# Kernel tuning notes

Measured on AMD Instinct MI355X. Metric: run time of the kernel, lower is better.

The kernel has to match this reference:

```python
import jax, jax.numpy as jnp
import numpy as np

HEADS = 8
HDIM = 64
MAX_PEMB = 512


def setup_inputs() -> dict:
    key = jax.random.key(0)
    ks = jax.random.split(key, 6)
    B, S, D = 4, 1024, 512
    return {
        "x": jax.random.normal(ks[0], (B, S, D), jnp.float32),
        "attn_mask": jnp.ones((B, S), jnp.bool_),
        "Wq": jax.random.normal(ks[1], (D, HEADS * HDIM), jnp.float32) * 0.02,
        "Wkv": jax.random.normal(ks[2], (D, 2 * HEADS * HDIM), jnp.float32) * 0.02,
        "Wout": jax.random.normal(ks[3], (HEADS * HDIM, D), jnp.float32) * 0.02,
        "bout": jnp.zeros((D,), jnp.float32),
        "pemb": jax.random.normal(ks[4], (2 * MAX_PEMB + 1, HDIM), jnp.float32) * 0.02,
    }


def reference(x, attn_mask, Wq, Wkv, Wout, bout, pemb):
    # attn_mask is unpacked but unused in the original call(); faithful to source.
    B, S, D = x.shape
    scale = HDIM ** (-0.5)

    q = (x @ Wq).reshape(B, S, HEADS, HDIM).transpose(0, 2, 1, 3)  # [B,H,S,hd]
    kv = x @ Wkv
    k, v = jnp.split(kv, 2, axis=-1)
    k = k.reshape(B, S, HEADS, HDIM).transpose(0, 2, 1, 3)
    v = v.reshape(B, S, HEADS, HDIM).transpose(0, 2, 1, 3)

    attn_score = jnp.einsum('bhqd,bhkd->bhqk', q, k) * scale

    seq = jnp.arange(S)
    dist = jnp.clip(seq[:, None] - seq[None, :], -MAX_PEMB, MAX_PEMB) + MAX_PEMB  # [S,S]
    rel_pemb = pemb[dist]  # [S,S,hd]
    pos_attn = jnp.einsum('bhsd,std->bhst', q, rel_pemb) * scale  # [B,H,S,S]

    attn_probs = jax.nn.softmax(attn_score + pos_attn, axis=-1)
    ctx = jnp.einsum('bhqk,bhkd->bqhd', attn_probs, v).reshape(B, S, HEADS * HDIM)
    return ctx @ Wout + bout
```

## Files before the change

### kernel.cpp

```cpp
#include <hip/hip_runtime.h>
#include <hip/hip_bf16.h>

constexpr int BATCH = 4;
constexpr int SEQ   = 1024;
constexpr int DM    = 512;
constexpr int NH    = 8;
constexpr int HD    = 64;
constexpr int NQKV  = 1536;

typedef unsigned short u16;
typedef __attribute__((ext_vector_type(8))) __bf16 bf8;
typedef __attribute__((ext_vector_type(4))) float  f4;

#define MFMA16(a, b, c) __builtin_amdgcn_mfma_f32_16x16x32_bf16(a, b, c, 0, 0, 0)

#define QSC 0.18033688f

static __device__ __forceinline__ u16 f2b(float f) {
    union { float f; unsigned u; } v; v.f = f;
    unsigned r = v.u + 0x7FFFu + ((v.u >> 16) & 1u);
    return (u16)(r >> 16);
}
static __device__ __forceinline__ float fexp2(float x) {
    return __builtin_amdgcn_exp2f(x);
}
static __device__ __forceinline__ void gl_lds16(const void* g, void* l) {
    __builtin_amdgcn_global_load_lds(
        (const __attribute__((address_space(1))) void*)g,
        (__attribute__((address_space(3))) void*)l, 16, 0, 0);
}

__device__ __forceinline__ void tcvt_tile(const float* __restrict__ in,
                                          u16* __restrict__ out,
                                          int R, int C, int bx, int by, int tid,
                                          float (*t)[33]) {
    int r0 = by * 32, c0 = bx * 32;
    int lc = tid & 31, lr = tid >> 5;
    #pragma unroll
    for (int p = 0; p < 4; p++) {
        int r = lr + p * 8;
        t[r][lc] = in[(size_t)(r0 + r) * C + c0 + lc];
    }
    __syncthreads();
    #pragma unroll
    for (int p = 0; p < 4; p++) {
        int r = lr + p * 8;
        out[(size_t)(c0 + r) * R + r0 + lc] = f2b(t[lc][r]);
    }
}

__global__ __launch_bounds__(256)
void prep(const float* __restrict__ x, const float* __restrict__ Wq,
          const float* __restrict__ Wkv, const float* __restrict__ Wout,
          const float* __restrict__ pemb,
          u16* __restrict__ xb, u16* __restrict__ qkvw,
          u16* __restrict__ Woutt, u16* __restrict__ pembb) {
    __shared__ float t[32][33];
    const int blk = blockIdx.x, tid = threadIdx.x;
    if (blk < 2048) {
        int i = (blk * 256 + tid) * 4;
        float4 v = *(const float4*)(x + i);
        ushort4 o = {f2b(v.x), f2b(v.y), f2b(v.z), f2b(v.w)};
        *(ushort4*)(xb + i) = o;
    } else if (blk < 2113) {
        int i = ((blk - 2048) * 256 + tid) * 4;
        if (i < 1025 * HD) {
            float4 v = *(const float4*)(pemb + i);
            ushort4 o = {f2b(v.x), f2b(v.y), f2b(v.z), f2b(v.w)};
            *(ushort4*)(pembb + i) = o;
        }
    } else if (blk < 2369) {
        int l = blk - 2113;
        tcvt_tile(Wq, qkvw, 512, 512, l & 15, l >> 4, tid, t);
    } else if (blk < 2881) {
        int l = blk - 2369;
        tcvt_tile(Wkv, qkvw + 512 * 512, 512, 1024, l & 31, l >> 5, tid, t);
    } else {
        int l = blk - 2881;
        tcvt_tile(Wout, Woutt, 512, 512, l & 15, l >> 4, tid, t);
    }
}

__global__ __launch_bounds__(256)
void gemm_bt(const u16* __restrict__ A, const u16* __restrict__ Bt,
             int M, int N, int K,
             float* __restrict__ Cf, const float* __restrict__ bias,
             __bf16* __restrict__ qtb, __bf16* __restrict__ ktb,
             __bf16* __restrict__ vtb) {
    __shared__ __align__(16) u16 As[2][64][32];
    __shared__ __align__(16) u16 Bs[2][128][32];
    const int tid = threadIdx.x, w = tid >> 6, lane = tid & 63;
    const int l15 = lane & 15, l4 = lane >> 4;
    const int wr = (w >> 1) * 32, wc = (w & 1) * 64;
    const int bm = blockIdx.y * 64, bn = blockIdx.x * 128;

    f4 acc[2][4];
    #pragma unroll
    for (int i = 0; i < 2; i++)
        #pragma unroll
        for (int j = 0; j < 4; j++) acc[i][j] = (f4){0.f, 0.f, 0.f, 0.f};

    const int rS = lane >> 2;
    const int cS = (lane & 3) * 8;

    for (int k0 = 0; k0 < K; k0 += 64) {
        #pragma unroll
        for (int ks = 0; ks < 2; ks++) {
            gl_lds16(A + (size_t)(bm + w * 16 + rS) * K + k0 + ks * 32 + cS,
                     &As[ks][w * 16][0]);
            gl_lds16(Bt + (size_t)(bn + w * 32 + rS) * K + k0 + ks * 32 + cS,
                     &Bs[ks][w * 32][0]);
            gl_lds16(Bt + (size_t)(bn + w * 32 + 16 + rS) * K + k0 + ks * 32 + cS,
                     &Bs[ks][w * 32 + 16][0]);
        }
        __syncthreads();
        #pragma unroll
        for (int ks = 0; ks < 2; ks++) {
            bf8 af[2], bf[4];
            #pragma unroll
            for (int i = 0; i < 2; i++)
                af[i] = *(const bf8*)&As[ks][wr + i * 16 + l15][l4 * 8];
            #pragma unroll
            for (int j = 0; j < 4; j++)
                bf[j] = *(const bf8*)&Bs[ks][wc + j * 16 + l15][l4 * 8];
            #pragma unroll
            for (int i = 0; i < 2; i++)
                #pragma unroll
                for (int j = 0; j < 4; j++)
                    acc[i][j] = MFMA16(af[i], bf[j], acc[i][j]);
        }
        __syncthreads();
    }
    #pragma unroll
    for (int i = 0; i < 2; i++)
        #pragma unroll
        for (int j = 0; j < 4; j++) {
            const int col = bn + wc + j * 16 + l15;
            const int row0 = bm + wr + i * 16 + l4 * 4;
            if (Cf) {
                #pragma unroll
                for (int reg = 0; reg < 4; reg++)
                    Cf[(size_t)(row0 + reg) * N + col] = acc[i][j][reg] + bias[col];
            } else if (col < 512) {
                int h = col >> 6, d = col & 63;
                #pragma unroll
                for (int reg = 0; reg < 4; reg++) {
                    int row = row0 + reg;
                    int b = row >> 10, t = row & 1023;
                    qtb[((((size_t)(b * 8 + h)) << 10 | t) << 6) | d] =
                        (__bf16)(acc[i][j][reg] * QSC);
                }
            } else if (col < 1024) {
                int h = (col >> 6) - 8, d = col & 63;
                #pragma unroll
                for (int reg = 0; reg < 4; reg++) {
                    int row = row0 + reg;
                    int b = row >> 10, t = row & 1023;
                    ktb[((((size_t)(b * 8 + h)) << 10 | t) << 6) | d] =
                        (__bf16)acc[i][j][reg];
                }
            } else {
                int h = (col >> 6) - 16, d = col & 63;
                int b = row0 >> 10, t = row0 & 1023;
                __bf16 pk[4];
                #pragma unroll
                for (int reg = 0; reg < 4; reg++) pk[reg] = (__bf16)acc[i][j][reg];
                *(ushort4*)&vtb[(((size_t)(b * 8 + h) * 64 + d) << 10) | t] =
                    *(ushort4*)pk;
            }
        }
}

__global__ __launch_bounds__(256)
void attn_mfma(const u16* __restrict__ qtb, const u16* __restrict__ ktb,
               const u16* __restrict__ vtb, const u16* __restrict__ pembb,
               __bf16* __restrict__ ctxb) {
    __shared__ __align__(16) __bf16 Kb[2][64][72];
    __shared__ __align__(16) __bf16 Vb[2][64][72];
    __shared__ __align__(16) __bf16 Ps[64][72];
    __shared__ __align__(16) __bf16 Qd[64][136];

    const int tid = threadIdx.x, w = tid >> 6, lane = tid & 63;
    const int l15 = lane & 15, l4 = lane >> 4;
    const int bh = blockIdx.x, b = bh >> 3;
    const int s0 = blockIdx.y * 64;

    const u16* qp = qtb + ((size_t)bh * SEQ + s0 + w * 16 + l15) * HD + l4 * 8;
    bf8 qa0 = *(const bf8*)qp;
    bf8 qa1 = *(const bf8*)(qp + 32);

    #pragma unroll
    for (int pass = 0; pass < 2; pass++) {
        const int jlo = s0 + 449 + pass * 64;
        #pragma unroll
        for (int jt = 0; jt < 4; jt++) {
            int jc = min(1024, max(0, jlo + jt * 16 + l15));
            const u16* pp = pembb + (size_t)jc * HD + l4 * 8;
            bf8 b0 = *(const bf8*)pp;
            bf8 b1 = *(const bf8*)(pp + 32);
            f4 f = (f4){0.f, 0.f, 0.f, 0.f};
            f = MFMA16(qa0, b0, f);
            f = MFMA16(qa1, b1, f);
            int sl = w * 16 + l4 * 4;
            int j = jlo + jt * 16 + l15;
            #pragma unroll
            for (int reg = 0; reg < 4; reg++)
                Qd[sl + reg][j & 127] = (__bf16)f[reg];
        }
    }
    asm volatile("" ::: "memory");

    float l_r[4] = {0.f, 0.f, 0.f, 0.f};
    f4 o[4];
    #pragma unroll
    for (int dt = 0; dt < 4; dt++) o[dt] = (f4){0.f, 0.f, 0.f, 0.f};

    const u16* kbase = ktb + (size_t)bh * SEQ * HD;
    const u16* vbase = vtb + (size_t)bh * HD * SEQ;
    const u16* pbase = pembb + l4 * 8;

    const int sr = tid >> 3, sc = (tid & 7) * 8;

    *(bf8*)&Kb[0][sr][sc]      = *(const bf8*)(kbase + (size_t)sr * HD + sc);
    *(bf8*)&Kb[0][sr + 32][sc] = *(const bf8*)(kbase + (size_t)(sr + 32) * HD + sc);
    *(bf8*)&Vb[0][sr][sc]      = *(const bf8*)(vbase + (size_t)sr * SEQ + sc);
    *(bf8*)&Vb[0][sr + 32][sc] = *(const bf8*)(vbase + (size_t)(sr + 32) * SEQ + sc);
    __syncthreads();

    for (int i = 0; i < 16; i++) {
        const int cur = i & 1, nxt = cur ^ 1;
        const int t0 = i * 64, t1 = t0 + 64;
        const bool pre = (i < 15);
        bf8 kr0, kr1, vr0, vr1, pb0[4], pb1[4];
        const int jlo_next = s0 + 449 - 64 * (i + 1);
        if (pre) {
            kr0 = *(const bf8*)(kbase + (size_t)(t1 + sr) * HD + sc);
            kr1 = *(const bf8*)(kbase + (size_t)(t1 + sr + 32) * HD + sc);
            vr0 = *(const bf8*)(vbase + (size_t)sr * SEQ + t1 + sc);
            vr1 = *(const bf8*)(vbase + (size_t)(sr + 32) * SEQ + t1 + sc);
            #pragma unroll
            for (int jt = 0; jt < 4; jt++) {
                int jc = min(1024, max(0, jlo_next + jt * 16 + l15));
                const u16* pp = pbase + (size_t)jc * HD;
                pb0[jt] = *(const bf8*)pp;
                pb1[jt] = *(const bf8*)(pp + 32);
            }
        }

        f4 s[4];
        #pragma unroll
        for (int jt = 0; jt < 4; jt++) {
            bf8 b0 = *(const bf8*)&Kb[cur][jt * 16 + l15][l4 * 8];
            bf8 b1 = *(const bf8*)&Kb[cur][jt * 16 + l15][32 + l4 * 8];
            f4 acc = (f4){0.f, 0.f, 0.f, 0.f};
            acc = MFMA16(qa0, b0, acc);
            acc = MFMA16(qa1, b1, acc);
            s[jt] = acc;
        }
        const int jbase = s0 - t0 + 512;
        float sc4[4][4];
        #pragma unroll
        for (int jt = 0; jt < 4; jt++) {
            int tl = jt * 16 + l15;
            #pragma unroll
            for (int reg = 0; reg < 4; reg++) {
                int sl = w * 16 + l4 * 4 + reg;
                int j = jbase + sl - tl;
                float p = fexp2(s[jt][reg] + (float)Qd[sl][j & 127]);
                sc4[jt][reg] = p;
                l_r[reg] += p;
            }
        }
        #pragma unroll
        for (int jt = 0; jt < 4; jt++)
            #pragma unroll
            for (int reg = 0; reg < 4; reg++)
                Ps[w * 16 + l4 * 4 + reg][jt * 16 + l15] = (__bf16)sc4[jt][reg];
        asm volatile("" ::: "memory");
        bf8 pa0 = *(const bf8*)&Ps[w * 16 + l15][l4 * 8];
        bf8 pa1 = *(const bf8*)&Ps[w * 16 + l15][32 + l4 * 8];
        #pragma unroll
        for (int dt = 0; dt < 4; dt++) {
            bf8 v0 = *(const bf8*)&Vb[cur][dt * 16 + l15][l4 * 8];
            bf8 v1 = *(const bf8*)&Vb[cur][dt * 16 + l15][32 + l4 * 8];
            o[dt] = MFMA16(pa0, v0, o[dt]);
            o[dt] = MFMA16(pa1, v1, o[dt]);
        }
        if (pre) {
            #pragma unroll
            for (int jt = 0; jt < 4; jt++) {
                f4 f = (f4){0.f, 0.f, 0.f, 0.f};
                f = MFMA16(qa0, pb0[jt], f);
                f = MFMA16(qa1, pb1[jt], f);
                int j = jlo_next + jt * 16 + l15;
                #pragma unroll
                for (int reg = 0; reg < 4; reg++)
                    Qd[w * 16 + l4 * 4 + reg][j & 127] = (__bf16)f[reg];
            }
            *(bf8*)&Kb[nxt][sr][sc]      = kr0;
            *(bf8*)&Kb[nxt][sr + 32][sc] = kr1;
            *(bf8*)&Vb[nxt][sr][sc]      = vr0;
            *(bf8*)&Vb[nxt][sr + 32][sc] = vr1;
        }
        __syncthreads();
    }
    #pragma unroll
    for (int reg = 0; reg < 4; reg++) {
        float r2 = l_r[reg];
        #pragma unroll
        for (int off = 8; off; off >>= 1) r2 += __shfl_xor(r2, off);
        l_r[reg] = 1.f / r2;
    }
    const int h = bh & 7;
    #pragma unroll
    for (int dt = 0; dt < 4; dt++)
        #pragma unroll
        for (int reg = 0; reg < 4; reg++) {
            int srow = s0 + w * 16 + l4 * 4 + reg;
            float v = o[dt][reg] * l_r[reg];
            ctxb[(size_t)(b * SEQ + srow) * DM + h * HD + dt * 16 + l15] = (__bf16)v;
        }
}

extern "C" void kernel_launch(void* const* d_in, const int* in_sizes, int n_in,
                              void* d_out, int out_size, void* d_ws, size_t ws_size,
                              hipStream_t stream) {
    const float* x    = (const float*)d_in[0];
    const float* Wq   = (const float*)d_in[2];
    const float* Wkv  = (const float*)d_in[3];
    const float* Wout = (const float*)d_in[4];
    const float* bout = (const float*)d_in[5];
    const float* pemb = (const float*)d_in[6];
    float* out = (float*)d_out;

    const int M = BATCH * SEQ;
    u16* p = (u16*)d_ws;
    u16* xb    = p; p += (size_t)M * DM;
    u16* qkvw  = p; p += (size_t)NQKV * DM;
    u16* Woutt = p; p += (size_t)DM * DM;
    u16* pembb = p; p += (size_t)1025 * HD;
    u16* qtb   = p; p += (size_t)M * DM;
    u16* ktb   = p; p += (size_t)M * DM;
    u16* vtb   = p; p += (size_t)M * DM;
    u16* ctxb  = p; p += (size_t)M * DM;

    prep<<<3137, 256, 0, stream>>>(x, Wq, Wkv, Wout, pemb, xb, qkvw, Woutt, pembb);

    gemm_bt<<<dim3(NQKV / 128, M / 64), 256, 0, stream>>>(
        xb, qkvw, M, NQKV, DM, nullptr, nullptr,
        (__bf16*)qtb, (__bf16*)ktb, (__bf16*)vtb);

    attn_mfma<<<dim3(BATCH * NH, SEQ / 64), 256, 0, stream>>>(
        qtb, ktb, vtb, pembb, (__bf16*)ctxb);

    gemm_bt<<<dim3(DM / 128, M / 64), 256, 0, stream>>>(
        ctxb, Woutt, M, DM, DM, out, bout, nullptr, nullptr, nullptr);
}
```

Before: 135.5 us.

## Load V fragments straight from global, swizzle P tile, deepen GEMM K-step

In the attention kernel, the V tile is no longer staged through shared memory. Each wave now loads its MFMA B-operand fragments for V directly from global memory on every iteration, which removes the Vb buffers and their LDS stores and reads. The P tile in shared memory now uses an XOR swizzle on columns to cut bank conflicts between the row-wise writes and the fragment reads. The QKV/out GEMM now stages 128 K-elements per barrier instead of 64, halving the number of syncs at the cost of twice the LDS footprint. The direct V loads are redundant across the four waves and are issued late, so they may expose global latency.

```diff
diff --git a/kernel.cpp b/kernel.cpp
--- a/kernel.cpp
+++ b/kernel.cpp
@@ -87,8 +87,8 @@
              float* __restrict__ Cf, const float* __restrict__ bias,
              __bf16* __restrict__ qtb, __bf16* __restrict__ ktb,
              __bf16* __restrict__ vtb) {
-    __shared__ __align__(16) u16 As[2][64][32];
-    __shared__ __align__(16) u16 Bs[2][128][32];
+    __shared__ __align__(16) u16 As[4][64][32];
+    __shared__ __align__(16) u16 Bs[4][128][32];
     const int tid = threadIdx.x, w = tid >> 6, lane = tid & 63;
     const int l15 = lane & 15, l4 = lane >> 4;
     const int wr = (w >> 1) * 32, wc = (w & 1) * 64;
@@ -103,9 +103,9 @@
     const int rS = lane >> 2;
     const int cS = (lane & 3) * 8;
 
-    for (int k0 = 0; k0 < K; k0 += 64) {
-        #pragma unroll
-        for (int ks = 0; ks < 2; ks++) {
+    for (int k0 = 0; k0 < K; k0 += 128) {
+        #pragma unroll
+        for (int ks = 0; ks < 4; ks++) {
             gl_lds16(A + (size_t)(bm + w * 16 + rS) * K + k0 + ks * 32 + cS,
                      &As[ks][w * 16][0]);
             gl_lds16(Bt + (size_t)(bn + w * 32 + rS) * K + k0 + ks * 32 + cS,
@@ -115,7 +115,7 @@
         }
         __syncthreads();
         #pragma unroll
-        for (int ks = 0; ks < 2; ks++) {
+        for (int ks = 0; ks < 4; ks++) {
             bf8 af[2], bf[4];
             #pragma unroll
             for (int i = 0; i < 2; i++)
@@ -176,7 +176,6 @@
                const u16* __restrict__ vtb, const u16* __restrict__ pembb,
                __bf16* __restrict__ ctxb) {
     __shared__ __align__(16) __bf16 Kb[2][64][72];
-    __shared__ __align__(16) __bf16 Vb[2][64][72];
     __shared__ __align__(16) __bf16 Ps[64][72];
     __shared__ __align__(16) __bf16 Qd[64][136];
 
@@ -184,6 +183,9 @@
     const int l15 = lane & 15, l4 = lane >> 4;
     const int bh = blockIdx.x, b = bh >> 3;
     const int s0 = blockIdx.y * 64;
+
+    const int xw = l4 << 4;
+    const int xr = (l15 >> 2) << 4;
 
     const u16* qp = qtb + ((size_t)bh * SEQ + s0 + w * 16 + l15) * HD + l4 * 8;
     bf8 qa0 = *(const bf8*)qp;
@@ -223,21 +225,17 @@
 
     *(bf8*)&Kb[0][sr][sc]      = *(const bf8*)(kbase + (size_t)sr * HD + sc);
     *(bf8*)&Kb[0][sr + 32][sc] = *(const bf8*)(kbase + (size_t)(sr + 32) * HD + sc);
-    *(bf8*)&Vb[0][sr][sc]      = *(const bf8*)(vbase + (size_t)sr * SEQ + sc);
-    *(bf8*)&Vb[0][sr + 32][sc] = *(const bf8*)(vbase + (size_t)(sr + 32) * SEQ + sc);
     __syncthreads();
 
     for (int i = 0; i < 16; i++) {
         const int cur = i & 1, nxt = cur ^ 1;
         const int t0 = i * 64, t1 = t0 + 64;
         const bool pre = (i < 15);
-        bf8 kr0, kr1, vr0, vr1, pb0[4], pb1[4];
+        bf8 kr0, kr1, pb0[4], pb1[4];
         const int jlo_next = s0 + 449 - 64 * (i + 1);
         if (pre) {
             kr0 = *(const bf8*)(kbase + (size_t)(t1 + sr) * HD + sc);
             kr1 = *(const bf8*)(kbase + (size_t)(t1 + sr + 32) * HD + sc);
-            vr0 = *(const bf8*)(vbase + (size_t)sr * SEQ + t1 + sc);
-            vr1 = *(const bf8*)(vbase + (size_t)(sr + 32) * SEQ + t1 + sc);
             #pragma unroll
             for (int jt = 0; jt < 4; jt++) {
                 int jc = min(1024, max(0, jlo_next + jt * 16 + l15));
@@ -257,6 +255,13 @@
             acc = MFMA16(qa1, b1, acc);
             s[jt] = acc;
         }
+        bf8 vf[4][2];
+        #pragma unroll
+        for (int dt = 0; dt < 4; dt++) {
+            const u16* vp = vbase + (size_t)(dt * 16 + l15) * SEQ + t0 + l4 * 8;
+            vf[dt][0] = *(const bf8*)vp;
+            vf[dt][1] = *(const bf8*)(vp + 32);
+        }
         const int jbase = s0 - t0 + 512;
         float sc4[4][4];
         #pragma unroll
@@ -275,16 +280,15 @@
         for (int jt = 0; jt < 4; jt++)
             #pragma unroll
             for (int reg = 0; reg < 4; reg++)
-                Ps[w * 16 + l4 * 4 + reg][jt * 16 + l15] = (__bf16)sc4[jt][reg];
+                Ps[w * 16 + l4 * 4 + reg][(jt * 16 + l15) ^ xw] =
+                    (__bf16)sc4[jt][reg];
         asm volatile("" ::: "memory");
-        bf8 pa0 = *(const bf8*)&Ps[w * 16 + l15][l4 * 8];
-        bf8 pa1 = *(const bf8*)&Ps[w * 16 + l15][32 + l4 * 8];
+        bf8 pa0 = *(const bf8*)&Ps[w * 16 + l15][(l4 * 8) ^ xr];
+        bf8 pa1 = *(const bf8*)&Ps[w * 16 + l15][(32 + l4 * 8) ^ xr];
         #pragma unroll
         for (int dt = 0; dt < 4; dt++) {
-            bf8 v0 = *(const bf8*)&Vb[cur][dt * 16 + l15][l4 * 8];
-            bf8 v1 = *(const bf8*)&Vb[cur][dt * 16 + l15][32 + l4 * 8];
-            o[dt] = MFMA16(pa0, v0, o[dt]);
-            o[dt] = MFMA16(pa1, v1, o[dt]);
+            o[dt] = MFMA16(pa0, vf[dt][0], o[dt]);
+            o[dt] = MFMA16(pa1, vf[dt][1], o[dt]);
         }
         if (pre) {
             #pragma unroll
@@ -299,8 +303,6 @@
             }
             *(bf8*)&Kb[nxt][sr][sc]      = kr0;
             *(bf8*)&Kb[nxt][sr + 32][sc] = kr1;
-            *(bf8*)&Vb[nxt][sr][sc]      = vr0;
-            *(bf8*)&Vb[nxt][sr + 32][sc] = vr1;
         }
         __syncthreads();
     }
```

After: 155.9 us. +15.1%, slower.

## Transpose Qd LDS layout, swizzle Ps columns, and hoist V fragment loads

Applied to the files above, without the earlier changes.

Stores the per-query relative-position table Qd transposed (position-major, 128x72) so each lane writes its four query rows as one packed 4-element store instead of four scalar stores. Applies an XOR swizzle to the Ps column index on both write and read to spread LDS bank accesses, and loads the V fragments from LDS before the softmax exponentials so their latency overlaps that math. The swizzled Ps reads and writes must agree exactly. The hoisted V fragments keep more values live in registers, which could lower occupancy.

```diff
diff --git a/kernel.cpp b/kernel.cpp
--- a/kernel.cpp
+++ b/kernel.cpp
@@ -10,6 +10,7 @@
 
 typedef unsigned short u16;
 typedef __attribute__((ext_vector_type(8))) __bf16 bf8;
+typedef __attribute__((ext_vector_type(4))) __bf16 bf4;
 typedef __attribute__((ext_vector_type(4))) float  f4;
 
 #define MFMA16(a, b, c) __builtin_amdgcn_mfma_f32_16x16x32_bf16(a, b, c, 0, 0, 0)
@@ -178,12 +179,17 @@
     __shared__ __align__(16) __bf16 Kb[2][64][72];
     __shared__ __align__(16) __bf16 Vb[2][64][72];
     __shared__ __align__(16) __bf16 Ps[64][72];
-    __shared__ __align__(16) __bf16 Qd[64][136];
+    __shared__ __align__(16) __bf16 Qd[128][72];
 
     const int tid = threadIdx.x, w = tid >> 6, lane = tid & 63;
     const int l15 = lane & 15, l4 = lane >> 4;
     const int bh = blockIdx.x, b = bh >> 3;
     const int s0 = blockIdx.y * 64;
+
+    const int xw = l4 << 4;
+    const int xr = (l15 >> 2) << 4;
+
+    const int sl0 = w * 16 + l4 * 4;
 
     const u16* qp = qtb + ((size_t)bh * SEQ + s0 + w * 16 + l15) * HD + l4 * 8;
     bf8 qa0 = *(const bf8*)qp;
@@ -201,11 +207,11 @@
             f4 f = (f4){0.f, 0.f, 0.f, 0.f};
             f = MFMA16(qa0, b0, f);
             f = MFMA16(qa1, b1, f);
-            int sl = w * 16 + l4 * 4;
             int j = jlo + jt * 16 + l15;
-            #pragma unroll
-            for (int reg = 0; reg < 4; reg++)
-                Qd[sl + reg][j & 127] = (__bf16)f[reg];
+            bf4 pk;
+            #pragma unroll
+            for (int reg = 0; reg < 4; reg++) pk[reg] = (__bf16)f[reg];
+            *(bf4*)&Qd[j & 127][sl0] = pk;
         }
     }
     asm volatile("" ::: "memory");
@@ -257,6 +263,12 @@
             acc = MFMA16(qa1, b1, acc);
             s[jt] = acc;
         }
+        bf8 vf0[4], vf1[4];
+        #pragma unroll
+        for (int dt = 0; dt < 4; dt++) {
+            vf0[dt] = *(const bf8*)&Vb[cur][dt * 16 + l15][l4 * 8];
+            vf1[dt] = *(const bf8*)&Vb[cur][dt * 16 + l15][32 + l4 * 8];
+        }
         const int jbase = s0 - t0 + 512;
         float sc4[4][4];
         #pragma unroll
@@ -264,9 +276,9 @@
             int tl = jt * 16 + l15;
             #pragma unroll
             for (int reg = 0; reg < 4; reg++) {
-                int sl = w * 16 + l4 * 4 + reg;
+                int sl = sl0 + reg;
                 int j = jbase + sl - tl;
-                float p = fexp2(s[jt][reg] + (float)Qd[sl][j & 127]);
+                float p = fexp2(s[jt][reg] + (float)Qd[j & 127][sl]);
                 sc4[jt][reg] = p;
                 l_r[reg] += p;
             }
@@ -275,16 +287,14 @@
         for (int jt = 0; jt < 4; jt++)
             #pragma unroll
             for (int reg = 0; reg < 4; reg++)
-                Ps[w * 16 + l4 * 4 + reg][jt * 16 + l15] = (__bf16)sc4[jt][reg];
+                Ps[sl0 + reg][(jt * 16 + l15) ^ xw] = (__bf16)sc4[jt][reg];
         asm volatile("" ::: "memory");
-        bf8 pa0 = *(const bf8*)&Ps[w * 16 + l15][l4 * 8];
-        bf8 pa1 = *(const bf8*)&Ps[w * 16 + l15][32 + l4 * 8];
+        bf8 pa0 = *(const bf8*)&Ps[w * 16 + l15][(l4 * 8) ^ xr];
+        bf8 pa1 = *(const bf8*)&Ps[w * 16 + l15][(32 + l4 * 8) ^ xr];
         #pragma unroll
         for (int dt = 0; dt < 4; dt++) {
-            bf8 v0 = *(const bf8*)&Vb[cur][dt * 16 + l15][l4 * 8];
-            bf8 v1 = *(const bf8*)&Vb[cur][dt * 16 + l15][32 + l4 * 8];
-            o[dt] = MFMA16(pa0, v0, o[dt]);
-            o[dt] = MFMA16(pa1, v1, o[dt]);
+            o[dt] = MFMA16(pa0, vf0[dt], o[dt]);
+            o[dt] = MFMA16(pa1, vf1[dt], o[dt]);
         }
         if (pre) {
             #pragma unroll
@@ -293,9 +303,10 @@
                 f = MFMA16(qa0, pb0[jt], f);
                 f = MFMA16(qa1, pb1[jt], f);
                 int j = jlo_next + jt * 16 + l15;
-                #pragma unroll
-                for (int reg = 0; reg < 4; reg++)
-                    Qd[w * 16 + l4 * 4 + reg][j & 127] = (__bf16)f[reg];
+                bf4 pk;
+                #pragma unroll
+                for (int reg = 0; reg < 4; reg++) pk[reg] = (__bf16)f[reg];
+                *(bf4*)&Qd[j & 127][sl0] = pk;
             }
             *(bf8*)&Kb[nxt][sr][sc]      = kr0;
             *(bf8*)&Kb[nxt][sr + 32][sc] = kr1;
```

After: 137.2 us. Within noise of the previous version (+1.2%).
